# Performance work log

Hardware: AMD Instinct MI355X
Metric: run time of the kernel (lower is better)

The kernel has to match this reference:

```python
import jax, jax.numpy as jnp
import numpy as np

C = 256
HEADS = 8
HEAD_DIM = C // HEADS
GROUPS = 8
EPS = 1e-5


def setup_inputs() -> dict:
    key = jax.random.key(0)
    ks = jax.random.split(key, 11)
    B, S = 2, 16
    s = 0.02
    return {
        "x": jax.random.normal(ks[0], (B, C, S, S, S), dtype=jnp.float32),
        "gn_w": jnp.ones((C,), jnp.float32),
        "gn_b": jnp.zeros((C,), jnp.float32),
        "wq": jax.random.normal(ks[1], (C, C), jnp.float32) * s,
        "bq": jnp.zeros((C,), jnp.float32),
        "wk": jax.random.normal(ks[2], (C, C), jnp.float32) * s,
        "bk": jnp.zeros((C,), jnp.float32),
        "wv": jax.random.normal(ks[3], (C, C), jnp.float32) * s,
        "bv": jnp.zeros((C,), jnp.float32),
        "wo": jax.random.normal(ks[4], (C, C), jnp.float32) * s,
        "bo": jnp.zeros((C,), jnp.float32),
    }


def _group_norm(x, w, b):
    # x: [B, C, D, H, W]; GroupNorm(8, C) with affine params
    B, Cc, D, H, W = x.shape
    xg = x.reshape(B, GROUPS, Cc // GROUPS, D, H, W)
    mu = jnp.mean(xg, axis=(2, 3, 4, 5), keepdims=True)
    var = jnp.mean(jnp.square(xg - mu), axis=(2, 3, 4, 5), keepdims=True)
    xn = ((xg - mu) * jax.lax.rsqrt(var + EPS)).reshape(B, Cc, D, H, W)
    return xn * w[None, :, None, None, None] + b[None, :, None, None, None]


def reference(x, gn_w, gn_b, wq, bq, wk, bk, wv, bv, wo, bo):
    B, Cc, D, H, W = x.shape
    N = D * H * W
    xn = _group_norm(x, gn_w, gn_b).reshape(B, Cc, N)  # [B,C,N]
    # 1x1x1 Conv3d == per-voxel linear: weight [out,in]
    Q = jnp.einsum("oc,bcn->bon", wq, xn) + bq[None, :, None]
    K = jnp.einsum("oc,bcn->bon", wk, xn) + bk[None, :, None]
    V = jnp.einsum("oc,bcn->bon", wv, xn) + bv[None, :, None]
    Q = Q.reshape(B, HEADS, HEAD_DIM, N)
    K = K.reshape(B, HEADS, HEAD_DIM, N)
    V = V.reshape(B, HEADS, HEAD_DIM, N)
    scale = np.sqrt(HEAD_DIM).astype(np.float32)
    attn = jnp.einsum("bhdn,bhdm->bhnm", Q, K) / scale
    attn = jax.nn.softmax(attn, axis=-1)
    out = jnp.einsum("bhnm,bhdm->bhdn", attn, V)  # [B,h,hd,N]
    out = out.reshape(B, Cc, N)
    out = jnp.einsum("oc,bcn->bon", wo, out) + bo[None, :, None]
    return x + out.reshape(B, Cc, D, H, W)
```

## Files before the change

### kernel.cpp

```cpp
#include <hip/hip_runtime.h>

#define B_   2
#define C_   256
#define N_   4096
#define H_   8
#define HD_  32
#define G_   8
#define CPG_ 32

typedef short short8 __attribute__((ext_vector_type(8)));
typedef float f32x4  __attribute__((ext_vector_type(4)));
typedef float f4     __attribute__((ext_vector_type(4)));

__device__ __forceinline__ float b2f(short s) {
    return __uint_as_float(((unsigned)(unsigned short)s) << 16);
}
__device__ __forceinline__ short f2b(float f) {
    unsigned u = __float_as_uint(f);
    unsigned r = (u + 0x7FFF + ((u >> 16) & 1)) >> 16;
    return (short)r;
}

__global__ __launch_bounds__(256) void gn_part(const float* __restrict__ x,
                                               float* __restrict__ part) {
    int blk = blockIdx.x;
    const f4* p = (const f4*)x + (size_t)(blk >> 6) * (CPG_ * N_ / 4) + (size_t)(blk & 63) * 512;
    float s = 0.f, ss = 0.f;
#pragma unroll
    for (int i = 0; i < 2; i++) {
        f4 v = p[threadIdx.x + i * 256];
#pragma unroll
        for (int j = 0; j < 4; j++) { float f = v[j]; s += f; ss += f * f; }
    }
#pragma unroll
    for (int off = 32; off > 0; off >>= 1) {
        s  += __shfl_down(s, off);
        ss += __shfl_down(ss, off);
    }
    __shared__ float rs[4], rss[4];
    int w = threadIdx.x >> 6;
    if ((threadIdx.x & 63) == 0) { rs[w] = s; rss[w] = ss; }
    __syncthreads();
    if (threadIdx.x == 0) {
        part[blk * 2]     = rs[0] + rs[1] + rs[2] + rs[3];
        part[blk * 2 + 1] = rss[0] + rss[1] + rss[2] + rss[3];
    }
}

__global__ __launch_bounds__(256) void gn_apply(const float* __restrict__ x,
                                                const float* __restrict__ gw,
                                                const float* __restrict__ gb,
                                                const float* __restrict__ part,
                                                short* __restrict__ xnT) {
    int t = blockIdx.x * 256 + threadIdx.x;
    int n  = t & 4095;
    int c0 = ((t >> 12) & 31) << 3;
    int b  = t >> 17;
    int g  = c0 >> 5;
    int bg = b * 8 + g;
    float s = 0.f, ss = 0.f;
#pragma unroll 8
    for (int i = 0; i < 64; i++) {
        s  += part[bg * 128 + i * 2];
        ss += part[bg * 128 + i * 2 + 1];
    }
    const float inv = 1.f / (float)(CPG_ * N_);
    float mu   = s * inv;
    float var  = ss * inv - mu * mu;
    float rstd = rsqrtf(var + 1e-5f);

    const float* xp = x + ((size_t)b * C_ + c0) * N_ + n;
    short8 o;
#pragma unroll
    for (int j = 0; j < 8; j++) {
        float a  = rstd * gw[c0 + j];
        float bb = gb[c0 + j] - mu * a;
        o[j] = f2b(xp[(size_t)j * N_] * a + bb);
    }
    *(short8*)&xnT[((size_t)b * N_ + n) * C_ + c0] = o;
}

__global__ __launch_bounds__(256) void gemm_qkv(
    const float* __restrict__ wq, const float* __restrict__ wk, const float* __restrict__ wv,
    const float* __restrict__ bq, const float* __restrict__ bk, const float* __restrict__ bv,
    const short* __restrict__ xnT,
    short* __restrict__ q, short* __restrict__ kt, short* __restrict__ v) {
    int z = blockIdx.z;
    int b = z / 3, which = z % 3;
    const float* W    = which == 0 ? wq : (which == 1 ? wk : wv);
    const float* bias = which == 0 ? bq : (which == 1 ? bk : bv);
    const short* X    = xnT + (size_t)b * N_ * C_;
    bool trans = (which != 2);
    float mul = (which == 0) ? (0.17677669529663687f * 1.4426950408889634f) : 1.0f;

    __shared__ short wl[64][40];
    __shared__ short xl[128][40];

    int o0 = blockIdx.y * 64, n0 = blockIdx.x * 128;
    int tid = threadIdx.x;
    int w = tid >> 6, lane = tid & 63, li = lane & 15, quad = lane >> 4;
    int wr = w & 1, wc = w >> 1;

    f32x4 acc[8];
#pragma unroll
    for (int i = 0; i < 8; i++) acc[i] = (f32x4){0.f, 0.f, 0.f, 0.f};

    for (int k0 = 0; k0 < 256; k0 += 32) {
        {
            int row = tid >> 2, co = (tid & 3) << 3;
            const float* wp = &W[(size_t)(o0 + row) * 256 + k0 + co];
            f4 wa = *(const f4*)wp;
            f4 wb = *(const f4*)(wp + 4);
            short8 w8;
#pragma unroll
            for (int j = 0; j < 4; j++) { w8[j] = f2b(wa[j]); w8[j + 4] = f2b(wb[j]); }
            *(short8*)&wl[row][co] = w8;
        }
#pragma unroll
        for (int i = 0; i < 2; i++) {
            int idx = tid + i * 256;
            int row = idx >> 2, co = (idx & 3) << 3;
            *(short8*)&xl[row][co] = *(const short8*)&X[(size_t)(n0 + row) * 256 + k0 + co];
        }
        __syncthreads();
        short8 af[4], bfr[4];
        if (trans) {
#pragma unroll
            for (int i = 0; i < 4; i++) af[i]  = *(short8*)&xl[wr * 64 + i * 16 + li][quad * 8];
#pragma unroll
            for (int j = 0; j < 2; j++) bfr[j] = *(short8*)&wl[wc * 32 + j * 16 + li][quad * 8];
#pragma unroll
            for (int i = 0; i < 4; i++)
#pragma unroll
                for (int j = 0; j < 2; j++)
                    acc[i * 2 + j] = __builtin_amdgcn_mfma_f32_16x16x32_bf16(af[i], bfr[j], acc[i * 2 + j], 0, 0, 0);
        } else {
#pragma unroll
            for (int i = 0; i < 2; i++) af[i]  = *(short8*)&wl[wr * 32 + i * 16 + li][quad * 8];
#pragma unroll
            for (int j = 0; j < 4; j++) bfr[j] = *(short8*)&xl[wc * 64 + j * 16 + li][quad * 8];
#pragma unroll
            for (int i = 0; i < 2; i++)
#pragma unroll
                for (int j = 0; j < 4; j++)
                    acc[i * 4 + j] = __builtin_amdgcn_mfma_f32_16x16x32_bf16(af[i], bfr[j], acc[i * 4 + j], 0, 0, 0);
        }
        __syncthreads();
    }

    if (which == 2) {
        short* outp = v + (size_t)b * C_ * N_;
#pragma unroll
        for (int i = 0; i < 2; i++) {
            int ob = o0 + wr * 32 + i * 16 + quad * 4;
#pragma unroll
            for (int j = 0; j < 4; j++) {
                int n_ = n0 + wc * 64 + j * 16 + li;
#pragma unroll
                for (int r = 0; r < 4; r++) {
                    float val = acc[i * 4 + j][r] + bias[ob + r];
                    outp[(size_t)(ob + r) * N_ + n_] = f2b(val);
                }
            }
        }
    } else if (which == 0) {
        short* outp = q + (size_t)b * N_ * C_;
#pragma unroll
        for (int i = 0; i < 4; i++) {
            int nb_ = n0 + wr * 64 + i * 16 + quad * 4;
#pragma unroll
            for (int j = 0; j < 2; j++) {
                int o_ = o0 + wc * 32 + j * 16 + li;
                float bv_ = bias[o_];
#pragma unroll
                for (int r = 0; r < 4; r++)
                    outp[(size_t)(nb_ + r) * C_ + o_] = f2b((acc[i * 2 + j][r] + bv_) * mul);
            }
        }
    } else {
#pragma unroll
        for (int i = 0; i < 4; i++) {
            int nb_ = n0 + wr * 64 + i * 16 + quad * 4;
#pragma unroll
            for (int j = 0; j < 2; j++) {
                int o_ = o0 + wc * 32 + j * 16 + li;
                int hh = o_ >> 5, d = o_ & 31;
                float bv_ = bias[o_];
                short* kdst = kt + ((size_t)(b * 8 + hh) * N_) * HD_ + d;
#pragma unroll
                for (int r = 0; r < 4; r++)
                    kdst[(size_t)(nb_ + r) * HD_] = f2b(acc[i * 2 + j][r] + bv_);
            }
        }
    }
}

#define STAGE_BARRIER(bufk, bufv)                                         \
    *(short8*)&kl[(bufk) * 2560 + klo] = kst;                             \
    *(short8*)&vl[(bufv) * 2304 + vlo] = vst;                             \
    __syncthreads();

#define PREFETCH(t1)                                                      \
    kst = *(const short8*)(kgp + (size_t)(t1) * 64 * HD_);                \
    vst = *(const short8*)(vgp + (t1) * 64);

#define LOADVF(vf, bufv)                                                  \
    vf[0] = *(short8*)&vl[(bufv) * 2304 + li * 72 + quad * 8];            \
    vf[1] = *(short8*)&vl[(bufv) * 2304 + (16 + li) * 72 + quad * 8];     \
    vf[2] = *(short8*)&vl[(bufv) * 2304 + li * 72 + 32 + quad * 8];       \
    vf[3] = *(short8*)&vl[(bufv) * 2304 + (16 + li) * 72 + 32 + quad * 8];

#define QK(bufk)                                                          \
    _Pragma("unroll")                                                     \
    for (int c = 0; c < 4; c++) {                                         \
        short8 kf = *(short8*)&kl[(bufk) * 2560 + (c * 16 + li) * 40 + quad * 8]; \
        s0[c] = __builtin_amdgcn_mfma_f32_16x16x32_bf16(kf, qf0, zero, 0, 0, 0);  \
        s1[c] = __builtin_amdgcn_mfma_f32_16x16x32_bf16(kf, qf1, zero, 0, 0, 0);  \
    }

#define PV(pP, vf)                                                        \
    {                                                                     \
        short8 pf00 = *(short8*)&(pP)[li * 72 + quad * 8];                \
        short8 pf01 = *(short8*)&(pP)[li * 72 + 32 + quad * 8];           \
        short8 pf10 = *(short8*)&(pP)[1152 + li * 72 + quad * 8];         \
        short8 pf11 = *(short8*)&(pP)[1152 + li * 72 + 32 + quad * 8];    \
        oa00 = __builtin_amdgcn_mfma_f32_16x16x32_bf16(pf00, vf[0], oa00, 0, 0, 0); \
        oa01 = __builtin_amdgcn_mfma_f32_16x16x32_bf16(pf00, vf[1], oa01, 0, 0, 0); \
        oa00 = __builtin_amdgcn_mfma_f32_16x16x32_bf16(pf01, vf[2], oa00, 0, 0, 0); \
        oa01 = __builtin_amdgcn_mfma_f32_16x16x32_bf16(pf01, vf[3], oa01, 0, 0, 0); \
        oa10 = __builtin_amdgcn_mfma_f32_16x16x32_bf16(pf10, vf[0], oa10, 0, 0, 0); \
        oa11 = __builtin_amdgcn_mfma_f32_16x16x32_bf16(pf10, vf[1], oa11, 0, 0, 0); \
        oa10 = __builtin_amdgcn_mfma_f32_16x16x32_bf16(pf11, vf[2], oa10, 0, 0, 0); \
        oa11 = __builtin_amdgcn_mfma_f32_16x16x32_bf16(pf11, vf[3], oa11, 0, 0, 0); \
    }

#define EXPPACK(pC)                                                       \
    {                                                                     \
        float lp = 0.f;                                                   \
        _Pragma("unroll")                                                 \
        for (int c = 0; c < 4; c++) {                                     \
            float e0 = __builtin_amdgcn_exp2f(s0[c][0]);                  \
            float e1 = __builtin_amdgcn_exp2f(s0[c][1]);                  \
            float e2 = __builtin_amdgcn_exp2f(s0[c][2]);                  \
            float e3 = __builtin_amdgcn_exp2f(s0[c][3]);                  \
            lp += (e0 + e1) + (e2 + e3);                                  \
            unsigned pk0 = __builtin_amdgcn_perm(__float_as_uint(e1), __float_as_uint(e0), 0x07060302); \
            unsigned pk1 = __builtin_amdgcn_perm(__float_as_uint(e3), __float_as_uint(e2), 0x07060302); \
            uint2 pkv; pkv.x = pk0; pkv.y = pk1;                          \
            *(uint2*)&(pC)[li * 72 + c * 16 + quad * 4] = pkv;            \
        }                                                                 \
        lr0 += lp;                                                        \
        lp = 0.f;                                                         \
        _Pragma("unroll")                                                 \
        for (int c = 0; c < 4; c++) {                                     \
            float e0 = __builtin_amdgcn_exp2f(s1[c][0]);                  \
            float e1 = __builtin_amdgcn_exp2f(s1[c][1]);                  \
            float e2 = __builtin_amdgcn_exp2f(s1[c][2]);                  \
            float e3 = __builtin_amdgcn_exp2f(s1[c][3]);                  \
            lp += (e0 + e1) + (e2 + e3);                                  \
            unsigned pk0 = __builtin_amdgcn_perm(__float_as_uint(e1), __float_as_uint(e0), 0x07060302); \
            unsigned pk1 = __builtin_amdgcn_perm(__float_as_uint(e3), __float_as_uint(e2), 0x07060302); \
            uint2 pkv; pkv.x = pk0; pkv.y = pk1;                          \
            *(uint2*)&(pC)[1152 + li * 72 + c * 16 + quad * 4] = pkv;     \
        }                                                                 \
        lr1 += lp;                                                        \
    }

__global__ __launch_bounds__(256) void flash(const short* __restrict__ q,
                                             const short* __restrict__ ktp,
                                             const short* __restrict__ v,
                                             short* __restrict__ aoT) {
    int bid = blockIdx.x;
    int xcd = bid & 7;
    int s_  = bid >> 3;
    int bh  = xcd * 2 + (s_ & 1);
    int nb  = s_ >> 1;
    int b = bh >> 3, h = bh & 7;

    const short* QT = q   + (size_t)b * N_ * C_ + h * HD_;
    const short* KP = ktp + (size_t)bh * N_ * HD_;
    const short* V  = v   + ((size_t)b * C_ + h * HD_) * N_;
    short* O = aoT + (size_t)b * N_ * C_ + h * HD_;

    __shared__ short kl[2 * 2560];
    __shared__ short vl[2 * 2304];
    __shared__ short pl[4 * 4608];

    int tid = threadIdx.x, w = tid >> 6, lane = tid & 63, li = lane & 15, quad = lane >> 4;
    int n0w = nb * 128 + w * 32;
    short* pA = pl + w * 4608;
    short* pB = pA + 2304;

    short8 qf0 = *(const short8*)&QT[(size_t)(n0w + li) * 256 + quad * 8];
    short8 qf1 = *(const short8*)&QT[(size_t)(n0w + 16 + li) * 256 + quad * 8];

    f32x4 oa00 = (f32x4){0.f,0.f,0.f,0.f}, oa01 = oa00, oa10 = oa00, oa11 = oa00;
    float lr0 = 0.f, lr1 = 0.f;
    const f32x4 zero = (f32x4){0.f, 0.f, 0.f, 0.f};

    int krow = tid >> 2, kcol = (tid & 3) << 3;
    int vrow = tid >> 3, vcol = (tid & 7) << 3;
    const short* kgp = KP + (size_t)krow * HD_ + kcol;
    const short* vgp = V + (size_t)vrow * N_ + vcol;
    int klo = krow * 40 + kcol;
    int vlo = vrow * 72 + vcol;

    short8 kst = *(const short8*)kgp;
    short8 vst = *(const short8*)vgp;
    short8 vfa[4], vfb[4];
    f32x4 s0[4], s1[4];

    STAGE_BARRIER(0, 0);
    PREFETCH(1);
    LOADVF(vfa, 0);
    QK(0);
    EXPPACK(pA);

    for (int mt = 1; mt < 62; mt += 2) {
        STAGE_BARRIER(1, 1);
        PREFETCH(mt + 1);
        LOADVF(vfb, 1);
        QK(1);
        PV(pA, vfa);
        EXPPACK(pB);
        STAGE_BARRIER(0, 0);
        PREFETCH(mt + 2);
        LOADVF(vfa, 0);
        QK(0);
        PV(pB, vfb);
        EXPPACK(pA);
    }
    STAGE_BARRIER(1, 1);
    LOADVF(vfb, 1);
    QK(1);
    PV(pA, vfa);
    EXPPACK(pB);
    PV(pB, vfb);

    lr0 += __shfl_xor(lr0, 16); lr0 += __shfl_xor(lr0, 32);
    lr1 += __shfl_xor(lr1, 16); lr1 += __shfl_xor(lr1, 32);
#pragma unroll
    for (int r2 = 0; r2 < 4; r2++) {
        float ln0 = __shfl(lr0, quad * 4 + r2);
        float inv0 = 1.f / ln0;
        size_t n_ = (size_t)(n0w + quad * 4 + r2);
        O[n_ * 256 + li]      = f2b(oa00[r2] * inv0);
        O[n_ * 256 + 16 + li] = f2b(oa01[r2] * inv0);
        float ln1 = __shfl(lr1, quad * 4 + r2);
        float inv1 = 1.f / ln1;
        size_t n2 = (size_t)(n0w + 16 + quad * 4 + r2);
        O[n2 * 256 + li]      = f2b(oa10[r2] * inv1);
        O[n2 * 256 + 16 + li] = f2b(oa11[r2] * inv1);
    }
}

__global__ __launch_bounds__(256) void gemm_out(const float* __restrict__ W,
                                                const float* __restrict__ bias,
                                                const short* __restrict__ aoT,
                                                const float* __restrict__ resid,
                                                float* __restrict__ out) {
    int b = blockIdx.z;
    const short* X = aoT + (size_t)b * N_ * C_;
    const float* R = resid + (size_t)b * C_ * N_;
    float* outp = out + (size_t)b * C_ * N_;

    __shared__ short wl[128][40];
    __shared__ short xl[64][40];

    int o0 = blockIdx.y * 128, n0 = blockIdx.x * 64;
    int tid = threadIdx.x;
    int w = tid >> 6, lane = tid & 63, li = lane & 15, quad = lane >> 4;
    int wr = w & 1, wc = w >> 1;

    f32x4 acc[4][2];
#pragma unroll
    for (int i = 0; i < 4; i++)
#pragma unroll
        for (int j = 0; j < 2; j++) acc[i][j] = (f32x4){0.f, 0.f, 0.f, 0.f};

    for (int k0 = 0; k0 < 256; k0 += 32) {
#pragma unroll
        for (int i = 0; i < 2; i++) {
            int idx = tid + i * 256;
            int row = idx >> 2, co = (idx & 3) << 3;
            const float* wp = &W[(size_t)(o0 + row) * 256 + k0 + co];
            f4 wa = *(const f4*)wp;
            f4 wb = *(const f4*)(wp + 4);
            short8 w8;
#pragma unroll
            for (int j = 0; j < 4; j++) { w8[j] = f2b(wa[j]); w8[j + 4] = f2b(wb[j]); }
            *(short8*)&wl[row][co] = w8;
        }
        {
            int row = tid >> 2, co = (tid & 3) << 3;
            *(short8*)&xl[row][co] = *(const short8*)&X[(size_t)(n0 + row) * 256 + k0 + co];
        }
        __syncthreads();
        short8 af[4], bfr[2];
#pragma unroll
        for (int i = 0; i < 4; i++) af[i]  = *(short8*)&wl[wr * 64 + i * 16 + li][quad * 8];
#pragma unroll
        for (int j = 0; j < 2; j++) bfr[j] = *(short8*)&xl[wc * 32 + j * 16 + li][quad * 8];
#pragma unroll
        for (int i = 0; i < 4; i++)
#pragma unroll
            for (int j = 0; j < 2; j++)
                acc[i][j] = __builtin_amdgcn_mfma_f32_16x16x32_bf16(af[i], bfr[j], acc[i][j], 0, 0, 0);
        __syncthreads();
    }
#pragma unroll
    for (int i = 0; i < 4; i++) {
        int ob = o0 + wr * 64 + i * 16 + quad * 4;
#pragma unroll
        for (int j = 0; j < 2; j++) {
            int n_ = n0 + wc * 32 + j * 16 + li;
#pragma unroll
            for (int r = 0; r < 4; r++) {
                size_t idx = (size_t)(ob + r) * N_ + n_;
                outp[idx] = acc[i][j][r] + bias[ob + r] + R[idx];
            }
        }
    }
}

extern "C" void kernel_launch(void* const* d_in, const int* in_sizes, int n_in,
                              void* d_out, int out_size, void* d_ws, size_t ws_size,
                              hipStream_t stream) {
    const float* x  = (const float*)d_in[0];
    const float* gw = (const float*)d_in[1];
    const float* gb = (const float*)d_in[2];
    const float* wq = (const float*)d_in[3];
    const float* bq = (const float*)d_in[4];
    const float* wk = (const float*)d_in[5];
    const float* bk = (const float*)d_in[6];
    const float* wv = (const float*)d_in[7];
    const float* bv = (const float*)d_in[8];
    const float* wo = (const float*)d_in[9];
    const float* bo = (const float*)d_in[10];
    float* out = (float*)d_out;

    char* ws = (char*)d_ws;
    float* part = (float*)ws;
    const size_t TS = (size_t)B_ * N_ * C_;
    short* xnT = (short*)(ws + 16384);
    short* q   = xnT + TS;
    short* kt  = q + TS;
    short* v   = kt + TS;
    short* aoT = xnT;

    gn_part<<<1024, 256, 0, stream>>>(x, part);
    gn_apply<<<1024, 256, 0, stream>>>(x, gw, gb, part, xnT);
    gemm_qkv<<<dim3(32, 4, 6), 256, 0, stream>>>(wq, wk, wv, bq, bk, bv, xnT, q, kt, v);
    flash<<<512, 256, 0, stream>>>(q, kt, v, aoT);
    gemm_out<<<dim3(64, 2, 2), 256, 0, stream>>>(wo, bo, aoT, x, out);
}
```

Before: 177.4 us.

## Fuse groupnorm apply into QKV GEMM and output projection into flash kernel

Group-norm statistics finalisation and normalisation move into the QKV GEMM's tile loader, which now reads fp32 x directly. This drops the gn_apply kernel and its bf16 xnT round trip. The output projection is merged into the flash kernel: the first 256 blocks, after finishing attention, spin on per-tile atomic counters until the 8 head-blocks covering their rows are done, then run the output GEMM. That saves two launches and their gaps. The cost is more global x traffic per QKV tile, since each o-tile re-normalises, plus strided scalar LDS stores, and the spin-wait relies on all producer blocks being co-resident or scheduled to avoid stalls or deadlock.

```diff
diff --git a/kernel.cpp b/kernel.cpp
--- a/kernel.cpp
+++ b/kernel.cpp
@@ -22,7 +22,9 @@
 }
 
 __global__ __launch_bounds__(256) void gn_part(const float* __restrict__ x,
-                                               float* __restrict__ part) {
+                                               float* __restrict__ part,
+                                               unsigned* __restrict__ cnt) {
+    if (blockIdx.x == 0 && threadIdx.x < 64) cnt[threadIdx.x] = 0u;
     int blk = blockIdx.x;
     const f4* p = (const f4*)x + (size_t)(blk >> 6) * (CPG_ * N_ / 4) + (size_t)(blk & 63) * 512;
     float s = 0.f, ss = 0.f;
@@ -47,63 +49,63 @@
     }
 }
 
-__global__ __launch_bounds__(256) void gn_apply(const float* __restrict__ x,
-                                                const float* __restrict__ gw,
-                                                const float* __restrict__ gb,
-                                                const float* __restrict__ part,
-                                                short* __restrict__ xnT) {
-    int t = blockIdx.x * 256 + threadIdx.x;
-    int n  = t & 4095;
-    int c0 = ((t >> 12) & 31) << 3;
-    int b  = t >> 17;
-    int g  = c0 >> 5;
-    int bg = b * 8 + g;
-    float s = 0.f, ss = 0.f;
-#pragma unroll 8
-    for (int i = 0; i < 64; i++) {
-        s  += part[bg * 128 + i * 2];
-        ss += part[bg * 128 + i * 2 + 1];
-    }
-    const float inv = 1.f / (float)(CPG_ * N_);
-    float mu   = s * inv;
-    float var  = ss * inv - mu * mu;
-    float rstd = rsqrtf(var + 1e-5f);
-
-    const float* xp = x + ((size_t)b * C_ + c0) * N_ + n;
-    short8 o;
-#pragma unroll
-    for (int j = 0; j < 8; j++) {
-        float a  = rstd * gw[c0 + j];
-        float bb = gb[c0 + j] - mu * a;
-        o[j] = f2b(xp[(size_t)j * N_] * a + bb);
-    }
-    *(short8*)&xnT[((size_t)b * N_ + n) * C_ + c0] = o;
-}
-
 __global__ __launch_bounds__(256) void gemm_qkv(
-    const float* __restrict__ wq, const float* __restrict__ wk, const float* __restrict__ wv,
-    const float* __restrict__ bq, const float* __restrict__ bk, const float* __restrict__ bv,
-    const short* __restrict__ xnT,
+    const float* __restrict__ x,
+    const float* __restrict__ gw, const float* __restrict__ gb,
+    const float* __restrict__ part,
+    const float* __restrict__ wq, const float* __restrict__ bq,
+    const float* __restrict__ wk, const float* __restrict__ bk,
+    const float* __restrict__ wv, const float* __restrict__ bv,
     short* __restrict__ q, short* __restrict__ kt, short* __restrict__ v) {
     int z = blockIdx.z;
     int b = z / 3, which = z % 3;
     const float* W    = which == 0 ? wq : (which == 1 ? wk : wv);
     const float* bias = which == 0 ? bq : (which == 1 ? bk : bv);
-    const short* X    = xnT + (size_t)b * N_ * C_;
     bool trans = (which != 2);
     float mul = (which == 0) ? (0.17677669529663687f * 1.4426950408889634f) : 1.0f;
 
     __shared__ short wl[64][40];
     __shared__ short xl[128][40];
+    __shared__ float ga[256], gbb[256];
+    __shared__ float mus[8], rstds[8];
 
     int o0 = blockIdx.y * 64, n0 = blockIdx.x * 128;
     int tid = threadIdx.x;
     int w = tid >> 6, lane = tid & 63, li = lane & 15, quad = lane >> 4;
     int wr = w & 1, wc = w >> 1;
 
+#pragma unroll
+    for (int gi = 0; gi < 2; gi++) {
+        int g = w * 2 + gi;
+        const float* pp = &part[(size_t)(b * 8 + g) * 128 + lane * 2];
+        float s = pp[0], ss = pp[1];
+#pragma unroll
+        for (int off = 32; off > 0; off >>= 1) {
+            s  += __shfl_down(s, off);
+            ss += __shfl_down(ss, off);
+        }
+        if (lane == 0) {
+            const float inv = 1.f / (float)(CPG_ * N_);
+            float mu = s * inv;
+            float var = ss * inv - mu * mu;
+            mus[g] = mu;
+            rstds[g] = rsqrtf(var + 1e-5f);
+        }
+    }
+    __syncthreads();
+    {
+        int c = tid, g = c >> 5;
+        float a = rstds[g] * gw[c];
+        ga[c]  = a;
+        gbb[c] = gb[c] - mus[g] * a;
+    }
+
     f32x4 acc[8];
 #pragma unroll
     for (int i = 0; i < 8; i++) acc[i] = (f32x4){0.f, 0.f, 0.f, 0.f};
+
+    int cc = tid & 31, nb8 = tid >> 5;
+    __syncthreads();
 
     for (int k0 = 0; k0 < 256; k0 += 32) {
         {
@@ -116,11 +118,23 @@
             for (int j = 0; j < 4; j++) { w8[j] = f2b(wa[j]); w8[j + 4] = f2b(wb[j]); }
             *(short8*)&wl[row][co] = w8;
         }
-#pragma unroll
-        for (int i = 0; i < 2; i++) {
-            int idx = tid + i * 256;
-            int row = idx >> 2, co = (idx & 3) << 3;
-            *(short8*)&xl[row][co] = *(const short8*)&X[(size_t)(n0 + row) * 256 + k0 + co];
+        {
+            float a  = ga[k0 + cc];
+            float bb = gbb[k0 + cc];
+            const float* xp = x + ((size_t)(b * 256 + k0 + cc)) * N_ + n0 + nb8 * 16;
+            f4 v0 = *(const f4*)xp;
+            f4 v1 = *(const f4*)(xp + 4);
+            f4 v2 = *(const f4*)(xp + 8);
+            f4 v3 = *(const f4*)(xp + 12);
+            int nbase = nb8 * 16;
+#pragma unroll
+            for (int j = 0; j < 4; j++) xl[nbase + j][cc]      = f2b(v0[j] * a + bb);
+#pragma unroll
+            for (int j = 0; j < 4; j++) xl[nbase + 4 + j][cc]  = f2b(v1[j] * a + bb);
+#pragma unroll
+            for (int j = 0; j < 4; j++) xl[nbase + 8 + j][cc]  = f2b(v2[j] * a + bb);
+#pragma unroll
+            for (int j = 0; j < 4; j++) xl[nbase + 12 + j][cc] = f2b(v3[j] * a + bb);
         }
         __syncthreads();
         short8 af[4], bfr[4];
@@ -266,158 +280,177 @@
         lr1 += lp;                                                        \
     }
 
-__global__ __launch_bounds__(256) void flash(const short* __restrict__ q,
-                                             const short* __restrict__ ktp,
-                                             const short* __restrict__ v,
-                                             short* __restrict__ aoT) {
+__global__ __launch_bounds__(256) void flash_out(const short* __restrict__ q,
+                                                 const short* __restrict__ ktp,
+                                                 const short* __restrict__ v,
+                                                 short* __restrict__ aoT,
+                                                 const float* __restrict__ wo,
+                                                 const float* __restrict__ bo,
+                                                 const float* __restrict__ resid,
+                                                 float* __restrict__ out,
+                                                 unsigned* __restrict__ cnt) {
+    __shared__ __align__(16) char smem[56320];
+    short* kl = (short*)smem;
+    short* vl = (short*)(smem + 10240);
+    short* pl = (short*)(smem + 19456);
+
     int bid = blockIdx.x;
-    int xcd = bid & 7;
-    int s_  = bid >> 3;
-    int bh  = xcd * 2 + (s_ & 1);
-    int nb  = s_ >> 1;
-    int b = bh >> 3, h = bh & 7;
-
-    const short* QT = q   + (size_t)b * N_ * C_ + h * HD_;
-    const short* KP = ktp + (size_t)bh * N_ * HD_;
-    const short* V  = v   + ((size_t)b * C_ + h * HD_) * N_;
-    short* O = aoT + (size_t)b * N_ * C_ + h * HD_;
-
-    __shared__ short kl[2 * 2560];
-    __shared__ short vl[2 * 2304];
-    __shared__ short pl[4 * 4608];
-
     int tid = threadIdx.x, w = tid >> 6, lane = tid & 63, li = lane & 15, quad = lane >> 4;
-    int n0w = nb * 128 + w * 32;
-    short* pA = pl + w * 4608;
-    short* pB = pA + 2304;
-
-    short8 qf0 = *(const short8*)&QT[(size_t)(n0w + li) * 256 + quad * 8];
-    short8 qf1 = *(const short8*)&QT[(size_t)(n0w + 16 + li) * 256 + quad * 8];
-
-    f32x4 oa00 = (f32x4){0.f,0.f,0.f,0.f}, oa01 = oa00, oa10 = oa00, oa11 = oa00;
-    float lr0 = 0.f, lr1 = 0.f;
-    const f32x4 zero = (f32x4){0.f, 0.f, 0.f, 0.f};
-
-    int krow = tid >> 2, kcol = (tid & 3) << 3;
-    int vrow = tid >> 3, vcol = (tid & 7) << 3;
-    const short* kgp = KP + (size_t)krow * HD_ + kcol;
-    const short* vgp = V + (size_t)vrow * N_ + vcol;
-    int klo = krow * 40 + kcol;
-    int vlo = vrow * 72 + vcol;
-
-    short8 kst = *(const short8*)kgp;
-    short8 vst = *(const short8*)vgp;
-    short8 vfa[4], vfb[4];
-    f32x4 s0[4], s1[4];
-
-    STAGE_BARRIER(0, 0);
-    PREFETCH(1);
-    LOADVF(vfa, 0);
-    QK(0);
-    EXPPACK(pA);
-
-    for (int mt = 1; mt < 62; mt += 2) {
+
+    {
+        int xcd = bid & 7;
+        int s_  = bid >> 3;
+        int bh  = xcd * 2 + (s_ & 1);
+        int nb  = s_ >> 1;
+        int b = bh >> 3, h = bh & 7;
+
+        const short* QT = q   + (size_t)b * N_ * C_ + h * HD_;
+        const short* KP = ktp + (size_t)bh * N_ * HD_;
+        const short* V  = v   + ((size_t)b * C_ + h * HD_) * N_;
+        short* O = aoT + (size_t)b * N_ * C_ + h * HD_;
+
+        int n0w = nb * 128 + w * 32;
+        short* pA = pl + w * 4608;
+        short* pB = pA + 2304;
+
+        short8 qf0 = *(const short8*)&QT[(size_t)(n0w + li) * 256 + quad * 8];
+        short8 qf1 = *(const short8*)&QT[(size_t)(n0w + 16 + li) * 256 + quad * 8];
+
+        f32x4 oa00 = (f32x4){0.f,0.f,0.f,0.f}, oa01 = oa00, oa10 = oa00, oa11 = oa00;
+        float lr0 = 0.f, lr1 = 0.f;
+        const f32x4 zero = (f32x4){0.f, 0.f, 0.f, 0.f};
+
+        int krow = tid >> 2, kcol = (tid & 3) << 3;
+        int vrow = tid >> 3, vcol = (tid & 7) << 3;
+        const short* kgp = KP + (size_t)krow * HD_ + kcol;
+        const short* vgp = V + (size_t)vrow * N_ + vcol;
+        int klo = krow * 40 + kcol;
+        int vlo = vrow * 72 + vcol;
+
+        short8 kst = *(const short8*)kgp;
+        short8 vst = *(const short8*)vgp;
+        short8 vfa[4], vfb[4];
+        f32x4 s0[4], s1[4];
+
+        STAGE_BARRIER(0, 0);
+        PREFETCH(1);
+        LOADVF(vfa, 0);
+        QK(0);
+        EXPPACK(pA);
+
+        for (int mt = 1; mt < 62; mt += 2) {
+            STAGE_BARRIER(1, 1);
+            PREFETCH(mt + 1);
+            LOADVF(vfb, 1);
+            QK(1);
+            PV(pA, vfa);
+            EXPPACK(pB);
+            STAGE_BARRIER(0, 0);
+            PREFETCH(mt + 2);
+            LOADVF(vfa, 0);
+            QK(0);
+            PV(pB, vfb);
+            EXPPACK(pA);
+        }
         STAGE_BARRIER(1, 1);
-        PREFETCH(mt + 1);
         LOADVF(vfb, 1);
         QK(1);
         PV(pA, vfa);
         EXPPACK(pB);
-        STAGE_BARRIER(0, 0);
-        PREFETCH(mt + 2);
-        LOADVF(vfa, 0);
-        QK(0);
         PV(pB, vfb);
-        EXPPACK(pA);
-    }
-    STAGE_BARRIER(1, 1);
-    LOADVF(vfb, 1);
-    QK(1);
-    PV(pA, vfa);
-    EXPPACK(pB);
-    PV(pB, vfb);
-
-    lr0 += __shfl_xor(lr0, 16); lr0 += __shfl_xor(lr0, 32);
-    lr1 += __shfl_xor(lr1, 16); lr1 += __shfl_xor(lr1, 32);
-#pragma unroll
-    for (int r2 = 0; r2 < 4; r2++) {
-        float ln0 = __shfl(lr0, quad * 4 + r2);
-        float inv0 = 1.f / ln0;
-        size_t n_ = (size_t)(n0w + quad * 4 + r2);
-        O[n_ * 256 + li]      = f2b(oa00[r2] * inv0);
-        O[n_ * 256 + 16 + li] = f2b(oa01[r2] * inv0);
-        float ln1 = __shfl(lr1, quad * 4 + r2);
-        float inv1 = 1.f / ln1;
-        size_t n2 = (size_t)(n0w + 16 + quad * 4 + r2);
-        O[n2 * 256 + li]      = f2b(oa10[r2] * inv1);
-        O[n2 * 256 + 16 + li] = f2b(oa11[r2] * inv1);
-    }
-}
-
-__global__ __launch_bounds__(256) void gemm_out(const float* __restrict__ W,
-                                                const float* __restrict__ bias,
-                                                const short* __restrict__ aoT,
-                                                const float* __restrict__ resid,
-                                                float* __restrict__ out) {
-    int b = blockIdx.z;
-    const short* X = aoT + (size_t)b * N_ * C_;
-    const float* R = resid + (size_t)b * C_ * N_;
-    float* outp = out + (size_t)b * C_ * N_;
-
-    __shared__ short wl[128][40];
-    __shared__ short xl[64][40];
-
-    int o0 = blockIdx.y * 128, n0 = blockIdx.x * 64;
-    int tid = threadIdx.x;
-    int w = tid >> 6, lane = tid & 63, li = lane & 15, quad = lane >> 4;
-    int wr = w & 1, wc = w >> 1;
-
-    f32x4 acc[4][2];
-#pragma unroll
-    for (int i = 0; i < 4; i++)
-#pragma unroll
-        for (int j = 0; j < 2; j++) acc[i][j] = (f32x4){0.f, 0.f, 0.f, 0.f};
-
-    for (int k0 = 0; k0 < 256; k0 += 32) {
-#pragma unroll
-        for (int i = 0; i < 2; i++) {
-            int idx = tid + i * 256;
-            int row = idx >> 2, co = (idx & 3) << 3;
-            const float* wp = &W[(size_t)(o0 + row) * 256 + k0 + co];
-            f4 wa = *(const f4*)wp;
-            f4 wb = *(const f4*)(wp + 4);
-            short8 w8;
-#pragma unroll
-            for (int j = 0; j < 4; j++) { w8[j] = f2b(wa[j]); w8[j + 4] = f2b(wb[j]); }
-            *(short8*)&wl[row][co] = w8;
-        }
-        {
-            int row = tid >> 2, co = (tid & 3) << 3;
-            *(short8*)&xl[row][co] = *(const short8*)&X[(size_t)(n0 + row) * 256 + k0 + co];
-        }
+
+        lr0 += __shfl_xor(lr0, 16); lr0 += __shfl_xor(lr0, 32);
+        lr1 += __shfl_xor(lr1, 16); lr1 += __shfl_xor(lr1, 32);
+#pragma unroll
+        for (int r2 = 0; r2 < 4; r2++) {
+            float ln0 = __shfl(lr0, quad * 4 + r2);
+            float inv0 = 1.f / ln0;
+            size_t n_ = (size_t)(n0w + quad * 4 + r2);
+            O[n_ * 256 + li]      = f2b(oa00[r2] * inv0);
+            O[n_ * 256 + 16 + li] = f2b(oa01[r2] * inv0);
+            float ln1 = __shfl(lr1, quad * 4 + r2);
+            float inv1 = 1.f / ln1;
+            size_t n2 = (size_t)(n0w + 16 + quad * 4 + r2);
+            O[n2 * 256 + li]      = f2b(oa10[r2] * inv1);
+            O[n2 * 256 + 16 + li] = f2b(oa11[r2] * inv1);
+        }
+
+        __threadfence();
         __syncthreads();
-        short8 af[4], bfr[2];
-#pragma unroll
-        for (int i = 0; i < 4; i++) af[i]  = *(short8*)&wl[wr * 64 + i * 16 + li][quad * 8];
-#pragma unroll
-        for (int j = 0; j < 2; j++) bfr[j] = *(short8*)&xl[wc * 32 + j * 16 + li][quad * 8];
+        if (tid == 0) atomicAdd(&cnt[b * 32 + nb], 1u);
+    }
+
+    if (bid >= 256) return;
+    {
+        int b  = bid >> 7;
+        int ot = (bid >> 6) & 1;
+        int nt = bid & 63;
+        int o0 = ot * 128, n0 = nt * 64;
+
+        if (tid == 0) {
+            unsigned* flag = &cnt[b * 32 + (nt >> 1)];
+            while (__hip_atomic_load(flag, __ATOMIC_ACQUIRE, __HIP_MEMORY_SCOPE_AGENT) < 8u)
+                __builtin_amdgcn_s_sleep(8);
+        }
+        __syncthreads();
+        __threadfence();
+
+        const short* X = aoT + (size_t)b * N_ * C_;
+        const float* R = resid + (size_t)b * C_ * N_;
+        float* outp = out + (size_t)b * C_ * N_;
+
+        typedef short row40[40];
+        row40* wl2 = (row40*)smem;
+        row40* xl2 = (row40*)(smem + 10240);
+
+        int wr = w & 1, wc = w >> 1;
+        f32x4 acc[4][2];
 #pragma unroll
         for (int i = 0; i < 4; i++)
 #pragma unroll
-            for (int j = 0; j < 2; j++)
-                acc[i][j] = __builtin_amdgcn_mfma_f32_16x16x32_bf16(af[i], bfr[j], acc[i][j], 0, 0, 0);
-        __syncthreads();
-    }
-#pragma unroll
-    for (int i = 0; i < 4; i++) {
-        int ob = o0 + wr * 64 + i * 16 + quad * 4;
-#pragma unroll
-        for (int j = 0; j < 2; j++) {
-            int n_ = n0 + wc * 32 + j * 16 + li;
-#pragma unroll
-            for (int r = 0; r < 4; r++) {
-                size_t idx = (size_t)(ob + r) * N_ + n_;
-                outp[idx] = acc[i][j][r] + bias[ob + r] + R[idx];
+            for (int j = 0; j < 2; j++) acc[i][j] = (f32x4){0.f, 0.f, 0.f, 0.f};
+
+        for (int k0 = 0; k0 < 256; k0 += 32) {
+#pragma unroll
+            for (int i = 0; i < 2; i++) {
+                int idx = tid + i * 256;
+                int row = idx >> 2, co = (idx & 3) << 3;
+                const float* wp = &wo[(size_t)(o0 + row) * 256 + k0 + co];
+                f4 wa = *(const f4*)wp;
+                f4 wb = *(const f4*)(wp + 4);
+                short8 w8;
+#pragma unroll
+                for (int j = 0; j < 4; j++) { w8[j] = f2b(wa[j]); w8[j + 4] = f2b(wb[j]); }
+                *(short8*)&wl2[row][co] = w8;
+            }
+            {
+                int row = tid >> 2, co = (tid & 3) << 3;
+                *(short8*)&xl2[row][co] = *(const short8*)&X[(size_t)(n0 + row) * 256 + k0 + co];
+            }
+            __syncthreads();
+            short8 af[4], bfr[2];
+#pragma unroll
+            for (int i = 0; i < 4; i++) af[i]  = *(short8*)&wl2[wr * 64 + i * 16 + li][quad * 8];
+#pragma unroll
+            for (int j = 0; j < 2; j++) bfr[j] = *(short8*)&xl2[wc * 32 + j * 16 + li][quad * 8];
+#pragma unroll
+            for (int i = 0; i < 4; i++)
+#pragma unroll
+                for (int j = 0; j < 2; j++)
+                    acc[i][j] = __builtin_amdgcn_mfma_f32_16x16x32_bf16(af[i], bfr[j], acc[i][j], 0, 0, 0);
+            __syncthreads();
+        }
+#pragma unroll
+        for (int i = 0; i < 4; i++) {
+            int ob = o0 + wr * 64 + i * 16 + quad * 4;
+#pragma unroll
+            for (int j = 0; j < 2; j++) {
+                int n_ = n0 + wc * 32 + j * 16 + li;
+#pragma unroll
+                for (int r = 0; r < 4; r++) {
+                    size_t idx = (size_t)(ob + r) * N_ + n_;
+                    outp[idx] = acc[i][j][r] + bo[ob + r] + R[idx];
+                }
             }
         }
     }
@@ -441,16 +474,15 @@
 
     char* ws = (char*)d_ws;
     float* part = (float*)ws;
+    unsigned* cnt = (unsigned*)(ws + 8192);
     const size_t TS = (size_t)B_ * N_ * C_;
-    short* xnT = (short*)(ws + 16384);
-    short* q   = xnT + TS;
+    short* aoT = (short*)(ws + 16384);
+    short* q   = aoT + TS;
     short* kt  = q + TS;
     short* v   = kt + TS;
-    short* aoT = xnT;
-
-    gn_part<<<1024, 256, 0, stream>>>(x, part);
-    gn_apply<<<1024, 256, 0, stream>>>(x, gw, gb, part, xnT);
-    gemm_qkv<<<dim3(32, 4, 6), 256, 0, stream>>>(wq, wk, wv, bq, bk, bv, xnT, q, kt, v);
-    flash<<<512, 256, 0, stream>>>(q, kt, v, aoT);
-    gemm_out<<<dim3(64, 2, 2), 256, 0, stream>>>(wo, bo, aoT, x, out);
-}
+
+    gn_part<<<1024, 256, 0, stream>>>(x, part, cnt);
+    gemm_qkv<<<dim3(32, 4, 6), 256, 0, stream>>>(x, gw, gb, part,
+                                                 wq, bq, wk, bk, wv, bv, q, kt, v);
+    flash_out<<<512, 256, 0, stream>>>(q, kt, v, aoT, wo, bo, x, out, cnt);
+}
```

Measured after the change: 274.6 us. 54.8% more time.
